# Optimization experiments

Measured on AMD Instinct MI355X. Metric: run time of the kernel, lower is better.

Reference implementation:

```python
import jax, jax.numpy as jnp
import numpy as np

N_WORDS, L_CHARS = 16384, 16
CHAR_SIZE, C_EMB = 128, 64
CONV_L, KERNEL, PAD = 256, 3, 2
VOCAB, D_EMB = 50000, 300
PAD_IDX = 1


def setup_inputs() -> dict:
    key = jax.random.key(0)
    k1, k2, k3, k4, k5, k6 = jax.random.split(key, 6)
    X = jax.random.randint(k1, (N_WORDS, L_CHARS), 0, CHAR_SIZE, dtype=jnp.int32)
    X_word = jax.random.randint(k2, (N_WORDS,), 0, VOCAB, dtype=jnp.int32)
    char_emb_w = jax.random.normal(k3, (CHAR_SIZE, C_EMB), dtype=jnp.float32)
    char_emb_w = char_emb_w.at[PAD_IDX].set(0.0)  # padding row zeroed, as in _init_char_embedding
    conv_w = jax.random.normal(k4, (CONV_L, C_EMB, KERNEL), dtype=jnp.float32) * 0.05
    conv_b = jax.random.normal(k5, (CONV_L,), dtype=jnp.float32) * 0.05
    word_emb_w = jax.random.normal(k6, (VOCAB, D_EMB), dtype=jnp.float32)
    return {"X": X, "X_word": X_word, "char_emb_w": char_emb_w,
            "conv_w": conv_w, "conv_b": conv_b, "word_emb_w": word_emb_w}


def reference(X, X_word, char_emb_w, conv_w, conv_b, word_emb_w):
    # char embedding lookup: [N, L, c_emb] -> NCH layout [N, c_emb, L]
    ce = char_emb_w[X].transpose(0, 2, 1)
    # Conv1d(c_emb -> conv_l, kernel=3, padding=2): out length L + 2*PAD - K + 1
    y = jax.lax.conv_general_dilated(
        ce, conv_w, window_strides=(1,), padding=[(PAD, PAD)],
        dimension_numbers=("NCH", "OIH", "NCH"))
    y = jax.nn.relu(y + conv_b[None, :, None])
    # MaxPool over the full time dimension -> [N, conv_l]
    char_feat = jnp.max(y, axis=2)
    # word embedding lookup: [N, d_emb]
    we = word_emb_w[X_word]
    return jnp.concatenate([char_feat, we], axis=1)
```

## Files before the change

kernel.cpp:

```cpp
#include <hip/hip_runtime.h>

#define N_WORDS   16384
#define L_CHARS   16
#define CHAR_SIZE 128
#define C_EMB     64
#define CONV_L    256
#define KERNEL_K  3
#define VOCAB     50000
#define D_EMB     300
#define OUT_STRIDE (CONV_L + D_EMB)

typedef _Float16 half8 __attribute__((ext_vector_type(8)));

__global__ void transpose_w(const float* __restrict__ w, float* __restrict__ Wt) {
    int tid = blockIdx.x * blockDim.x + threadIdx.x;
    if (tid >= CONV_L * C_EMB * KERNEL_K) return;
    int o = tid / (C_EMB * KERNEL_K);
    int r = tid - o * (C_EMB * KERNEL_K);
    int i = r / KERNEL_K;
    int k = r - i * KERNEL_K;
    Wt[i * (KERNEL_K * CONV_L) + k * CONV_L + o] = w[tid];
}

__global__ void build_table(const float* __restrict__ emb,
                            const float* __restrict__ Wt,
                            _Float16* __restrict__ Th) {
    int c  = blockIdx.x / 3;
    int ko = (blockIdx.x % 3) * 256 + threadIdx.x;
    const float* erow = emb + c * C_EMB;
    float s = 0.f;
    #pragma unroll
    for (int i = 0; i < C_EMB; ++i)
        s += erow[i] * Wt[i * (KERNEL_K * CONV_L) + ko];
    Th[c * (KERNEL_K * CONV_L) + ko] = (_Float16)s;
}

__global__ __launch_bounds__(256, 4)
void main_kernel(const int* __restrict__ X,
                 const int* __restrict__ Xw,
                 const _Float16* __restrict__ Th,
                 const float* __restrict__ conv_b,
                 const float* __restrict__ word_emb,
                 float* __restrict__ out,
                 int word_blocks, int char_blocks) {
    const int lane = threadIdx.x & 63;
    const int waveInBlock = threadIdx.x >> 6;

    if ((int)blockIdx.x < word_blocks) {
        const int wavesTotal = word_blocks * 4;
        const int waveId = blockIdx.x * 4 + waveInBlock;
        for (int n = waveId; n < N_WORDS; n += wavesTotal) {
            int widx = Xw[n];
            const float4* src = (const float4*)(word_emb + (size_t)widx * D_EMB);
            float4* dst = (float4*)(out + (size_t)n * OUT_STRIDE + CONV_L);
            dst[lane] = src[lane];
            if (lane < (D_EMB / 4 - 64)) {
                dst[64 + lane] = src[64 + lane];
            }
        }
    } else {
        const int wavesTotal = char_blocks * 4;
        const int waveId = ((int)blockIdx.x - word_blocks) * 4 + waveInBlock;
        const int sel = lane >> 5;
        const int l32 = lane & 31;

        float bias[8];
        {
            float4 b0 = ((const float4*)(conv_b + l32 * 8))[0];
            float4 b1 = ((const float4*)(conv_b + l32 * 8))[1];
            bias[0]=b0.x; bias[1]=b0.y; bias[2]=b0.z; bias[3]=b0.w;
            bias[4]=b1.x; bias[5]=b1.y; bias[6]=b1.z; bias[7]=b1.w;
        }

        for (int p = waveId; p < N_WORDS / 2; p += wavesTotal) {
            const int n = p * 2 + sel;
            const int4* xr = (const int4*)(X + n * L_CHARS);
            int4 q0 = xr[0], q1 = xr[1], q2 = xr[2], q3 = xr[3];
            int cs[16] = {q0.x, q0.y, q0.z, q0.w,
                          q1.x, q1.y, q1.z, q1.w,
                          q2.x, q2.y, q2.z, q2.w,
                          q3.x, q3.y, q3.z, q3.w};

            float a0[8], a1[8], m[8];
            #pragma unroll
            for (int e = 0; e < 8; ++e) { a0[e] = 0.f; a1[e] = 0.f; m[e] = -1e30f; }

            #pragma unroll
            for (int j = 0; j < L_CHARS; ++j) {
                const half8* Tc = (const half8*)(Th + cs[j] * (KERNEL_K * CONV_L));
                half8 t0 = Tc[l32];
                half8 t1 = Tc[32 + l32];
                half8 t2 = Tc[64 + l32];
                #pragma unroll
                for (int e = 0; e < 8; ++e) {
                    float yj = a0[e] + (float)t2[e];
                    m[e]  = fmaxf(m[e], yj);
                    a0[e] = a1[e] + (float)t1[e];
                    a1[e] = (float)t0[e];
                }
            }
            float4 r0, r1;
            float r[8];
            #pragma unroll
            for (int e = 0; e < 8; ++e) {
                float mm = fmaxf(fmaxf(m[e], a0[e]), a1[e]);
                r[e] = fmaxf(mm + bias[e], 0.f);
            }
            r0 = make_float4(r[0], r[1], r[2], r[3]);
            r1 = make_float4(r[4], r[5], r[6], r[7]);
            float4* dst = (float4*)(out + (size_t)n * OUT_STRIDE + l32 * 8);
            dst[0] = r0;
            dst[1] = r1;
        }
    }
}

extern "C" void kernel_launch(void* const* d_in, const int* in_sizes, int n_in,
                              void* d_out, int out_size, void* d_ws, size_t ws_size,
                              hipStream_t stream) {
    const int*   X    = (const int*)d_in[0];
    const int*   Xw   = (const int*)d_in[1];
    const float* emb  = (const float*)d_in[2];
    const float* w    = (const float*)d_in[3];
    const float* b    = (const float*)d_in[4];
    const float* we   = (const float*)d_in[5];
    float* out = (float*)d_out;

    _Float16* Th = (_Float16*)d_ws;
    float*    Wt = (float*)((char*)d_ws + CHAR_SIZE * KERNEL_K * CONV_L * sizeof(_Float16));

    transpose_w<<<(CONV_L * C_EMB * KERNEL_K + 255) / 256, 256, 0, stream>>>(w, Wt);
    build_table<<<CHAR_SIZE * KERNEL_K, 256, 0, stream>>>(emb, Wt, Th);

    const int WB = 256;
    const int CB = 1024;
    main_kernel<<<WB + CB, 256, 0, stream>>>(X, Xw, Th, b, we, out, WB, CB);
}
```

Baseline: 135.9 us.

## Use packed fp16 accumulation, double-buffer table loads, drop weight transpose kernel

The char-conv inner loop now keeps the sliding accumulators and the running max in half8 vectors, using packed fp16 adds and max instead of per-element fp32 converts. Table rows are loaded four characters at a time into two alternating register buffers so loads overlap with compute. The separate weight-transpose launch is removed, and build_table reads the original conv weights directly with strided access. Occupancy is lowered to 3 blocks per SIMD to make room for the extra registers. fp16 accumulation of three taps adds some rounding error.

```diff
diff --git a/kernel.cpp b/kernel.cpp
--- a/kernel.cpp
+++ b/kernel.cpp
@@ -6,36 +6,39 @@
 #define C_EMB     64
 #define CONV_L    256
 #define KERNEL_K  3
-#define VOCAB     50000
 #define D_EMB     300
 #define OUT_STRIDE (CONV_L + D_EMB)
+#define T_ROW     (KERNEL_K * CONV_L)
 
 typedef _Float16 half8 __attribute__((ext_vector_type(8)));
 
-__global__ void transpose_w(const float* __restrict__ w, float* __restrict__ Wt) {
-    int tid = blockIdx.x * blockDim.x + threadIdx.x;
-    if (tid >= CONV_L * C_EMB * KERNEL_K) return;
-    int o = tid / (C_EMB * KERNEL_K);
-    int r = tid - o * (C_EMB * KERNEL_K);
-    int i = r / KERNEL_K;
-    int k = r - i * KERNEL_K;
-    Wt[i * (KERNEL_K * CONV_L) + k * CONV_L + o] = w[tid];
+static __device__ __forceinline__ half8 h8max(half8 a, half8 b) {
+#if __has_builtin(__builtin_elementwise_max)
+    return __builtin_elementwise_max(a, b);
+#else
+    half8 r;
+    #pragma unroll
+    for (int i = 0; i < 8; ++i) r[i] = a[i] > b[i] ? a[i] : b[i];
+    return r;
+#endif
 }
 
 __global__ void build_table(const float* __restrict__ emb,
-                            const float* __restrict__ Wt,
+                            const float* __restrict__ w,
                             _Float16* __restrict__ Th) {
-    int c  = blockIdx.x / 3;
-    int ko = (blockIdx.x % 3) * 256 + threadIdx.x;
+    int c = blockIdx.x / 3;
+    int k = blockIdx.x % 3;
+    int o = threadIdx.x;
     const float* erow = emb + c * C_EMB;
+    const float* wrow = w + o * (C_EMB * KERNEL_K) + k;
     float s = 0.f;
     #pragma unroll
     for (int i = 0; i < C_EMB; ++i)
-        s += erow[i] * Wt[i * (KERNEL_K * CONV_L) + ko];
-    Th[c * (KERNEL_K * CONV_L) + ko] = (_Float16)s;
+        s += erow[i] * wrow[i * KERNEL_K];
+    Th[c * T_ROW + k * CONV_L + o] = (_Float16)s;
 }
 
-__global__ __launch_bounds__(256, 4)
+__global__ __launch_bounds__(256, 3)
 void main_kernel(const int* __restrict__ X,
                  const int* __restrict__ Xw,
                  const _Float16* __restrict__ Th,
@@ -81,36 +84,52 @@
                           q2.x, q2.y, q2.z, q2.w,
                           q3.x, q3.y, q3.z, q3.w};
 
-            float a0[8], a1[8], m[8];
-            #pragma unroll
-            for (int e = 0; e < 8; ++e) { a0[e] = 0.f; a1[e] = 0.f; m[e] = -1e30f; }
+            half8 A[4][3], B[4][3];
+            half8 a0 = (half8)(_Float16)0.f;
+            half8 a1 = (half8)(_Float16)0.f;
+            half8 m  = (half8)(_Float16)(-65504.f);
 
-            #pragma unroll
-            for (int j = 0; j < L_CHARS; ++j) {
-                const half8* Tc = (const half8*)(Th + cs[j] * (KERNEL_K * CONV_L));
-                half8 t0 = Tc[l32];
-                half8 t1 = Tc[32 + l32];
-                half8 t2 = Tc[64 + l32];
-                #pragma unroll
-                for (int e = 0; e < 8; ++e) {
-                    float yj = a0[e] + (float)t2[e];
-                    m[e]  = fmaxf(m[e], yj);
-                    a0[e] = a1[e] + (float)t1[e];
-                    a1[e] = (float)t0[e];
-                }
+#define LOADG(BUF, G)                                                      \
+            {                                                              \
+                _Pragma("unroll")                                          \
+                for (int jj = 0; jj < 4; ++jj) {                           \
+                    const half8* Tc =                                      \
+                        (const half8*)(Th + cs[(G) * 4 + jj] * T_ROW);     \
+                    BUF[jj][0] = Tc[l32];                                  \
+                    BUF[jj][1] = Tc[32 + l32];                             \
+                    BUF[jj][2] = Tc[64 + l32];                             \
+                }                                                          \
             }
-            float4 r0, r1;
+#define COMPG(BUF)                                                         \
+            {                                                              \
+                _Pragma("unroll")                                          \
+                for (int jj = 0; jj < 4; ++jj) {                           \
+                    half8 yj = a0 + BUF[jj][2];                            \
+                    m  = h8max(m, yj);                                     \
+                    a0 = a1 + BUF[jj][1];                                  \
+                    a1 = BUF[jj][0];                                       \
+                }                                                          \
+            }
+            LOADG(A, 0);
+            LOADG(B, 1);
+            COMPG(A);
+            LOADG(A, 2);
+            COMPG(B);
+            LOADG(B, 3);
+            COMPG(A);
+            COMPG(B);
+#undef LOADG
+#undef COMPG
+            m = h8max(m, a0);
+            m = h8max(m, a1);
+
             float r[8];
             #pragma unroll
-            for (int e = 0; e < 8; ++e) {
-                float mm = fmaxf(fmaxf(m[e], a0[e]), a1[e]);
-                r[e] = fmaxf(mm + bias[e], 0.f);
-            }
-            r0 = make_float4(r[0], r[1], r[2], r[3]);
-            r1 = make_float4(r[4], r[5], r[6], r[7]);
+            for (int e = 0; e < 8; ++e)
+                r[e] = fmaxf((float)m[e] + bias[e], 0.f);
             float4* dst = (float4*)(out + (size_t)n * OUT_STRIDE + l32 * 8);
-            dst[0] = r0;
-            dst[1] = r1;
+            dst[0] = make_float4(r[0], r[1], r[2], r[3]);
+            dst[1] = make_float4(r[4], r[5], r[6], r[7]);
         }
     }
 }
@@ -127,10 +146,8 @@
     float* out = (float*)d_out;
 
     _Float16* Th = (_Float16*)d_ws;
-    float*    Wt = (float*)((char*)d_ws + CHAR_SIZE * KERNEL_K * CONV_L * sizeof(_Float16));
 
-    transpose_w<<<(CONV_L * C_EMB * KERNEL_K + 255) / 256, 256, 0, stream>>>(w, Wt);
-    build_table<<<CHAR_SIZE * KERNEL_K, 256, 0, stream>>>(emb, Wt, Th);
+    build_table<<<CHAR_SIZE * KERNEL_K, 256, 0, stream>>>(emb, w, Th);
 
     const int WB = 256;
     const int CB = 1024;
```

Result: slower. 147.9 us (+8.8%).

## Stage per-channel-quarter conv table slices in LDS and accumulate in packed fp16

Applied to the files above, without the earlier changes.

The precomputed char-by-tap table is re-laid out into four 64-channel slices. Each char block copies one 48 KB slice into shared memory and processes 64 words for that channel quarter, so the 16 per-word gathers hit LDS instead of global/L2. The running sums and max are now kept as packed half8 vectors rather than unpacked to fp32, which cuts ALU work but adds fp16 rounding on accumulated values. Launch bounds drop to 3 blocks per CU to fit the larger shared memory footprint, and the word-embedding blocks also allocate the unused LDS.

```diff
diff --git a/kernel.cpp b/kernel.cpp
--- a/kernel.cpp
+++ b/kernel.cpp
@@ -6,11 +6,23 @@
 #define C_EMB     64
 #define CONV_L    256
 #define KERNEL_K  3
-#define VOCAB     50000
 #define D_EMB     300
 #define OUT_STRIDE (CONV_L + D_EMB)
+#define CH_Q      64
+#define SLICE_H   (CHAR_SIZE * KERNEL_K * CH_Q)
 
 typedef _Float16 half8 __attribute__((ext_vector_type(8)));
+
+static __device__ __forceinline__ half8 h8max(half8 a, half8 b) {
+#if __has_builtin(__builtin_elementwise_max)
+    return __builtin_elementwise_max(a, b);
+#else
+    half8 r;
+    #pragma unroll
+    for (int i = 0; i < 8; ++i) r[i] = a[i] > b[i] ? a[i] : b[i];
+    return r;
+#endif
+}
 
 __global__ void transpose_w(const float* __restrict__ w, float* __restrict__ Wt) {
     int tid = blockIdx.x * blockDim.x + threadIdx.x;
@@ -25,30 +37,35 @@
 __global__ void build_table(const float* __restrict__ emb,
                             const float* __restrict__ Wt,
                             _Float16* __restrict__ Th) {
-    int c  = blockIdx.x / 3;
-    int ko = (blockIdx.x % 3) * 256 + threadIdx.x;
+    int c = blockIdx.x / 3;
+    int k = blockIdx.x % 3;
+    int o = threadIdx.x;
     const float* erow = emb + c * C_EMB;
     float s = 0.f;
     #pragma unroll
     for (int i = 0; i < C_EMB; ++i)
-        s += erow[i] * Wt[i * (KERNEL_K * CONV_L) + ko];
-    Th[c * (KERNEL_K * CONV_L) + ko] = (_Float16)s;
+        s += erow[i] * Wt[i * (KERNEL_K * CONV_L) + k * CONV_L + o];
+    int q  = o >> 6;
+    int oi = o & 63;
+    Th[q * SLICE_H + c * (KERNEL_K * CH_Q) + k * CH_Q + oi] = (_Float16)s;
 }
 
-__global__ __launch_bounds__(256, 4)
+__global__ __launch_bounds__(256, 3)
 void main_kernel(const int* __restrict__ X,
                  const int* __restrict__ Xw,
                  const _Float16* __restrict__ Th,
                  const float* __restrict__ conv_b,
                  const float* __restrict__ word_emb,
                  float* __restrict__ out,
-                 int word_blocks, int char_blocks) {
+                 int word_blocks) {
+    __shared__ __align__(16) _Float16 Ts[SLICE_H];
+
     const int lane = threadIdx.x & 63;
-    const int waveInBlock = threadIdx.x >> 6;
+    const int wv   = threadIdx.x >> 6;
 
     if ((int)blockIdx.x < word_blocks) {
         const int wavesTotal = word_blocks * 4;
-        const int waveId = blockIdx.x * 4 + waveInBlock;
+        const int waveId = blockIdx.x * 4 + wv;
         for (int n = waveId; n < N_WORDS; n += wavesTotal) {
             int widx = Xw[n];
             const float4* src = (const float4*)(word_emb + (size_t)widx * D_EMB);
@@ -58,60 +75,69 @@
                 dst[64 + lane] = src[64 + lane];
             }
         }
-    } else {
-        const int wavesTotal = char_blocks * 4;
-        const int waveId = ((int)blockIdx.x - word_blocks) * 4 + waveInBlock;
-        const int sel = lane >> 5;
-        const int l32 = lane & 31;
+        return;
+    }
 
-        float bias[8];
-        {
-            float4 b0 = ((const float4*)(conv_b + l32 * 8))[0];
-            float4 b1 = ((const float4*)(conv_b + l32 * 8))[1];
-            bias[0]=b0.x; bias[1]=b0.y; bias[2]=b0.z; bias[3]=b0.w;
-            bias[4]=b1.x; bias[5]=b1.y; bias[6]=b1.z; bias[7]=b1.w;
+    const int cb   = (int)blockIdx.x - word_blocks;
+    const int q    = cb & 3;
+    const int wgrp = cb >> 2;
+
+    {
+        const float4* src = (const float4*)(Th + q * SLICE_H);
+        float4* dst = (float4*)Ts;
+        #pragma unroll
+        for (int i = 0; i < 12; ++i)
+            dst[threadIdx.x + i * 256] = src[threadIdx.x + i * 256];
+    }
+    __syncthreads();
+
+    const int g  = lane >> 3;
+    const int l8 = lane & 7;
+
+    float bias[8];
+    {
+        const float4* bp = (const float4*)(conv_b + q * CH_Q + l8 * 8);
+        float4 b0 = bp[0], b1 = bp[1];
+        bias[0]=b0.x; bias[1]=b0.y; bias[2]=b0.z; bias[3]=b0.w;
+        bias[4]=b1.x; bias[5]=b1.y; bias[6]=b1.z; bias[7]=b1.w;
+    }
+
+    #pragma unroll
+    for (int pass = 0; pass < 2; ++pass) {
+        const int n = wgrp * 64 + pass * 32 + wv * 8 + g;
+
+        const int4* xr = (const int4*)(X + n * L_CHARS);
+        int4 q0 = xr[0], q1 = xr[1], q2 = xr[2], q3 = xr[3];
+        int cs[16] = {q0.x, q0.y, q0.z, q0.w,
+                      q1.x, q1.y, q1.z, q1.w,
+                      q2.x, q2.y, q2.z, q2.w,
+                      q3.x, q3.y, q3.z, q3.w};
+
+        half8 a0 = (half8)(_Float16)0.f;
+        half8 a1 = (half8)(_Float16)0.f;
+        half8 m  = (half8)(_Float16)(-65504.f);
+
+        #pragma unroll
+        for (int j = 0; j < L_CHARS; ++j) {
+            const _Float16* row = Ts + cs[j] * (KERNEL_K * CH_Q) + l8 * 8;
+            half8 t0 = *(const half8*)(row);
+            half8 t1 = *(const half8*)(row + CH_Q);
+            half8 t2 = *(const half8*)(row + 2*CH_Q);
+            half8 yj = a0 + t2;
+            m  = h8max(m, yj);
+            a0 = a1 + t1;
+            a1 = t0;
         }
+        m = h8max(m, a0);
+        m = h8max(m, a1);
 
-        for (int p = waveId; p < N_WORDS / 2; p += wavesTotal) {
-            const int n = p * 2 + sel;
-            const int4* xr = (const int4*)(X + n * L_CHARS);
-            int4 q0 = xr[0], q1 = xr[1], q2 = xr[2], q3 = xr[3];
-            int cs[16] = {q0.x, q0.y, q0.z, q0.w,
-                          q1.x, q1.y, q1.z, q1.w,
-                          q2.x, q2.y, q2.z, q2.w,
-                          q3.x, q3.y, q3.z, q3.w};
-
-            float a0[8], a1[8], m[8];
-            #pragma unroll
-            for (int e = 0; e < 8; ++e) { a0[e] = 0.f; a1[e] = 0.f; m[e] = -1e30f; }
-
-            #pragma unroll
-            for (int j = 0; j < L_CHARS; ++j) {
-                const half8* Tc = (const half8*)(Th + cs[j] * (KERNEL_K * CONV_L));
-                half8 t0 = Tc[l32];
-                half8 t1 = Tc[32 + l32];
-                half8 t2 = Tc[64 + l32];
-                #pragma unroll
-                for (int e = 0; e < 8; ++e) {
-                    float yj = a0[e] + (float)t2[e];
-                    m[e]  = fmaxf(m[e], yj);
-                    a0[e] = a1[e] + (float)t1[e];
-                    a1[e] = (float)t0[e];
-                }
-            }
-            float4 r0, r1;
-            float r[8];
-            #pragma unroll
-            for (int e = 0; e < 8; ++e) {
-                float mm = fmaxf(fmaxf(m[e], a0[e]), a1[e]);
-                r[e] = fmaxf(mm + bias[e], 0.f);
-            }
-            r0 = make_float4(r[0], r[1], r[2], r[3]);
-            r1 = make_float4(r[4], r[5], r[6], r[7]);
-            float4* dst = (float4*)(out + (size_t)n * OUT_STRIDE + l32 * 8);
-            dst[0] = r0;
-            dst[1] = r1;
-        }
+        float r[8];
+        #pragma unroll
+        for (int e = 0; e < 8; ++e)
+            r[e] = fmaxf((float)m[e] + bias[e], 0.f);
+        float4* dst = (float4*)(out + (size_t)n * OUT_STRIDE + q * CH_Q + l8 * 8);
+        dst[0] = make_float4(r[0], r[1], r[2], r[3]);
+        dst[1] = make_float4(r[4], r[5], r[6], r[7]);
     }
 }
 
@@ -127,12 +153,12 @@
     float* out = (float*)d_out;
 
     _Float16* Th = (_Float16*)d_ws;
-    float*    Wt = (float*)((char*)d_ws + CHAR_SIZE * KERNEL_K * CONV_L * sizeof(_Float16));
+    float*    Wt = (float*)((char*)d_ws + 4 * SLICE_H * sizeof(_Float16));
 
     transpose_w<<<(CONV_L * C_EMB * KERNEL_K + 255) / 256, 256, 0, stream>>>(w, Wt);
     build_table<<<CHAR_SIZE * KERNEL_K, 256, 0, stream>>>(emb, Wt, Th);
 
     const int WB = 256;
     const int CB = 1024;
-    main_kernel<<<WB + CB, 256, 0, stream>>>(X, Xw, Th, b, we, out, WB, CB);
+    main_kernel<<<WB + CB, 256, 0, stream>>>(X, Xw, Th, b, we, out, WB);
 }
```

New measurement: 134.4 us (median of 2 runs). Within noise of the previous version (-1.2%).
